# Performance work log

Hardware: AMD Instinct MI355X
Metric: run time of the kernel (lower is better)

Reference implementation:

```python
import jax, jax.numpy as jnp
import numpy as np

B, DIM, IMG, HEADS, DH = 8, 512, 32, 8, 64
INNER = HEADS * DH  # == DIM, required by final reshape(b, n, c)
N = IMG * IMG
BN_EPS = 1e-5


def setup_inputs() -> dict:
    key = jax.random.key(0)
    ks = jax.random.split(key, 11)
    s = lambda k, sh: jax.random.normal(k, sh, jnp.float32) * 0.05
    return {
        "x": jax.random.normal(ks[0], (B, N, DIM), jnp.float32),
        # stacked q/k/v params, index 0=q, 1=k, 2=v
        "dw_w": s(ks[1], (3, DIM, 1, 3, 3)),   # depthwise conv kernels (OIHW, groups=DIM)
        "dw_b": s(ks[2], (3, DIM)),
        "bn_g": jnp.ones((3, DIM), jnp.float32) + s(ks[3], (3, DIM)),
        "bn_b": s(ks[4], (3, DIM)),
        "bn_m": s(ks[5], (3, DIM)),
        "bn_v": jnp.abs(jax.random.normal(ks[6], (3, DIM), jnp.float32)) + 1.0,
        "pw_w": s(ks[7], (3, INNER, DIM)),     # pointwise 1x1 conv weights
        "pw_b": s(ks[8], (3, INNER)),
        "out_w": s(ks[9], (DIM, INNER)),       # nn.Linear weight [out, in]
        "out_b": s(ks[10], (DIM,)),
    }


def _proj(x_img, dw_w, dw_b, bn_g, bn_b, bn_m, bn_v, pw_w, pw_b):
    # depthwise 3x3 conv, stride 1, pad 1
    y = jax.lax.conv_general_dilated(
        x_img, dw_w, (1, 1), [(1, 1), (1, 1)],
        dimension_numbers=("NCHW", "OIHW", "NCHW"), feature_group_count=DIM)
    y = y + dw_b[None, :, None, None]
    # eval-mode BatchNorm2d
    scale = bn_g / jnp.sqrt(bn_v + BN_EPS)
    y = (y - bn_m[None, :, None, None]) * scale[None, :, None, None] + bn_b[None, :, None, None]
    # pointwise 1x1 conv
    y = jnp.einsum("bchw,oc->bohw", y, pw_w) + pw_b[None, :, None, None]
    return y


def reference(x, dw_w, dw_b, bn_g, bn_b, bn_m, bn_v, pw_w, pw_b, out_w, out_b):
    b = x.shape[0]
    # b (l w) c -> b c l w
    xi = x.transpose(0, 2, 1).reshape(b, DIM, IMG, IMG)
    # q, k, v: b (h d) l w -> b h (l w) d
    qkv = [
        _proj(xi, dw_w[i], dw_b[i], bn_g[i], bn_b[i], bn_m[i], bn_v[i], pw_w[i], pw_b[i])
        .reshape(b, HEADS, DH, N).transpose(0, 1, 3, 2)
        for i in range(3)
    ]
    q, k, v = qkv
    att = jax.nn.softmax(jnp.einsum("bhnd,bhmd->bhnm", q, k) * (DH ** -0.5), axis=-1)
    out = jnp.einsum("bhnm,bhmd->bhnd", att, v)  # [b,h,n,d]
    out = out.transpose(0, 2, 1, 3).reshape(b, N, INNER)
    return out @ out_w.T + out_b  # to_out Linear (dropout=0)
```

## Files before the change

### kernel.cpp

```cpp
#include <hip/hip_runtime.h>
#include <hip/hip_bf16.h>

#define BB    8
#define DIMC  512
#define IMGS  32
#define NPIX  1024
#define NHEAD 8
#define DHEAD 64

typedef __attribute__((ext_vector_type(8))) short short8;
typedef __attribute__((ext_vector_type(4))) float float4v;

__device__ __forceinline__ float b2f(unsigned short u) {
  union { unsigned int i; float f; } c;
  c.i = ((unsigned int)u) << 16;
  return c.f;
}
__device__ __forceinline__ unsigned short f2b(float f) {
  union { float f; unsigned int u; } c;
  c.f = f;
  unsigned int r = c.u + 0x7fffu + ((c.u >> 16) & 1u);
  return (unsigned short)(r >> 16);
}

__device__ __forceinline__ void storeC(float* p, float v) { *p = v; }
__device__ __forceinline__ void storeC(unsigned short* p, float v) { *p = f2b(v); }

__device__ __forceinline__ void async16(const void* g, void* l) {
  __builtin_amdgcn_global_load_lds(
      (const __attribute__((address_space(1))) void*)g,
      (__attribute__((address_space(3))) void*)l, 16, 0, 0);
}

#define WAITCNT_VM0   0x0F70
#define WAITCNT_LGKM0 0xC07F

__global__ __launch_bounds__(256) void wcvt_kernel(
    const float* __restrict__ pw_w, const float* __restrict__ out_w,
    const float* __restrict__ pw_b, const float* __restrict__ dw_w,
    const float* __restrict__ dw_b, const float* __restrict__ bn_g,
    const float* __restrict__ bn_b, const float* __restrict__ bn_m,
    const float* __restrict__ bn_v, unsigned short* __restrict__ wbf,
    float* __restrict__ bb, float* __restrict__ wT,
    float* __restrict__ shiftv) {
  const int i4 = (blockIdx.x * 256 + threadIdx.x) * 4;
  float4 v = (i4 < 3 * DIMC * DIMC)
                 ? *reinterpret_cast<const float4*>(pw_w + i4)
                 : *reinterpret_cast<const float4*>(out_w + (i4 - 3 * DIMC * DIMC));
  const float sc = (i4 < DIMC * DIMC) ? 0.125f : 1.0f;
  ushort4 o;
  o.x = f2b(v.x * sc); o.y = f2b(v.y * sc); o.z = f2b(v.z * sc); o.w = f2b(v.w * sc);
  *reinterpret_cast<ushort4*>(wbf + i4) = o;
  const int idx = blockIdx.x * 256 + threadIdx.x;
  if (idx < 6 * 256) {
    if (idx < 3 * DIMC / 2) {
      #pragma unroll
      for (int hh = 0; hh < 2; ++hh) {
        const int id2 = idx * 2 + hh;
        const int i = id2 >> 9, c = id2 & 511;
        const float scale = bn_g[id2] * rsqrtf(bn_v[id2] + 1e-5f);
        shiftv[id2] = (dw_b[id2] - bn_m[id2]) * scale + bn_b[id2];
        #pragma unroll
        for (int t = 0; t < 9; ++t)
          wT[(i * 9 + t) * DIMC + c] = dw_w[(size_t)id2 * 9 + t] * scale;
      }
    }
    #pragma unroll
    for (int k = 0; k < 1; ++k) {
      if (idx < 3 * DIMC)
        bb[idx] = pw_b[idx] * (idx < DIMC ? 0.125f : 1.0f);
    }
  }
}

__global__ __launch_bounds__(256) void dwbn_kernel(
    const float* __restrict__ x, const float* __restrict__ wT,
    const float* __restrict__ shiftv, unsigned short* __restrict__ z) {
  const int wp = blockIdx.x, lg = blockIdx.y, b = blockIdx.z;
  const int t = threadIdx.x;
  const int c = (t & 127) * 4;
  const int w = wp * 2 + (t >> 7);
  const int l0 = lg * 4;
  const float* xb = x + (size_t)b * NPIX * DIMC + c;

  const float4 zero4 = make_float4(0.f, 0.f, 0.f, 0.f);
  float4 win[6][3];
  #pragma unroll
  for (int rr = 0; rr < 6; ++rr) {
    const int l = l0 - 1 + rr;
    #pragma unroll
    for (int dw = 0; dw < 3; ++dw) {
      const int ww = w - 1 + dw;
      const bool ok = ((unsigned)l < IMGS) && ((unsigned)ww < IMGS);
      win[rr][dw] = ok ? *reinterpret_cast<const float4*>(
                             xb + (size_t)(l * IMGS + ww) * DIMC)
                       : zero4;
    }
  }

  #pragma unroll
  for (int i = 0; i < 3; ++i) {
    float4 wv[9];
    #pragma unroll
    for (int tp = 0; tp < 9; ++tp)
      wv[tp] = *reinterpret_cast<const float4*>(wT + (i * 9 + tp) * DIMC + c);
    const float4 sh = *reinterpret_cast<const float4*>(shiftv + i * DIMC + c);
    #pragma unroll
    for (int r = 0; r < 4; ++r) {
      float a0 = sh.x, a1 = sh.y, a2 = sh.z, a3 = sh.w;
      #pragma unroll
      for (int kh = 0; kh < 3; ++kh)
        #pragma unroll
        for (int kw = 0; kw < 3; ++kw) {
          const float4 wq = wv[kh * 3 + kw];
          const float4 xq = win[r + kh][kw];
          a0 = fmaf(wq.x, xq.x, a0);
          a1 = fmaf(wq.y, xq.y, a1);
          a2 = fmaf(wq.z, xq.z, a2);
          a3 = fmaf(wq.w, xq.w, a3);
        }
      ushort4 st;
      st.x = f2b(a0); st.y = f2b(a1); st.z = f2b(a2); st.w = f2b(a3);
      *reinterpret_cast<ushort4*>(
          z + (((size_t)(i * BB + b)) * NPIX + (l0 + r) * IMGS + w) * DIMC + c) = st;
    }
  }
}

template <typename CT>
__global__ __launch_bounds__(256) void gemm_mfma(
    const unsigned short* __restrict__ Abase,
    const unsigned short* __restrict__ Wbase,
    const float* __restrict__ biasBase, CT* __restrict__ Cbase) {
  __shared__ short As[8 * 64 * 8];
  __shared__ short Bs[8 * 64 * 8];
  const int bz = blockIdx.z;
  const int wi = bz >> 3;
  const short* A = (const short*)Abase + (size_t)bz * NPIX * DIMC;
  const short* W = (const short*)Wbase + (size_t)wi * DIMC * DIMC;
  const float* bias = biasBase + wi * DIMC;
  CT* C = Cbase + (size_t)bz * NPIX * DIMC;

  const int t = threadIdx.x;
  const int wv = t >> 6, lane = t & 63;
  const int lo = lane & 15, hi = lane >> 4;
  const int wm = wv >> 1, wn = wv & 1;
  const int m0 = blockIdx.y * 128, n0 = blockIdx.x * 128;

  float4v acc[4][4];
  #pragma unroll
  for (int i = 0; i < 4; ++i)
    #pragma unroll
    for (int j = 0; j < 4; ++j) acc[i][j] = {0.f, 0.f, 0.f, 0.f};

  for (int k0 = 0; k0 < DIMC; k0 += 32) {
    #pragma unroll
    for (int p = 0; p < 2; ++p) {
      const int sub = wv + p * 4;
      async16(A + (size_t)(m0 + sub * 16 + lo) * DIMC + k0 + hi * 8,
              As + (sub * 64 + lane) * 8);
      async16(W + (size_t)(n0 + sub * 16 + lo) * DIMC + k0 + hi * 8,
              Bs + (sub * 64 + lane) * 8);
    }
    __syncthreads();
    short8 af[4], bf[4];
    #pragma unroll
    for (int mt = 0; mt < 4; ++mt)
      af[mt] = *reinterpret_cast<const short8*>(As + ((wm * 4 + mt) * 64 + lane) * 8);
    #pragma unroll
    for (int nt = 0; nt < 4; ++nt)
      bf[nt] = *reinterpret_cast<const short8*>(Bs + ((wn * 4 + nt) * 64 + lane) * 8);
    #pragma unroll
    for (int mt = 0; mt < 4; ++mt)
      #pragma unroll
      for (int nt = 0; nt < 4; ++nt)
        acc[mt][nt] = __builtin_amdgcn_mfma_f32_16x16x32_bf16(af[mt], bf[nt],
                                                              acc[mt][nt], 0, 0, 0);
    __syncthreads();
  }

  float bv[4];
  #pragma unroll
  for (int nt = 0; nt < 4; ++nt) bv[nt] = bias[n0 + wn * 64 + nt * 16 + lo];
  #pragma unroll
  for (int mt = 0; mt < 4; ++mt) {
    #pragma unroll
    for (int r = 0; r < 4; ++r) {
      const int row = m0 + wm * 64 + mt * 16 + hi * 4 + r;
      CT* cp = C + (size_t)row * DIMC + n0 + wn * 64 + lo;
      #pragma unroll
      for (int nt = 0; nt < 4; ++nt) storeC(cp + nt * 16, acc[mt][nt][r] + bv[nt]);
    }
  }
}

__global__ __launch_bounds__(256) void vt_kernel(
    const unsigned short* __restrict__ v, unsigned short* __restrict__ vt) {
  __shared__ unsigned short tile[64][68];
  const int n0 = blockIdx.x * 64, h = blockIdx.y, b = blockIdx.z;
  const int t = threadIdx.x;
  const unsigned short* vb = v + (size_t)b * NPIX * DIMC + h * DHEAD;
  #pragma unroll
  for (int u = 0; u < 4; ++u) {
    const int lin = t + u * 256;
    const int row = lin >> 4, c4 = (lin & 15) * 4;
    *reinterpret_cast<ushort4*>(&tile[row][c4]) =
        *reinterpret_cast<const ushort4*>(vb + (size_t)(n0 + row) * DIMC + c4);
  }
  __syncthreads();
  unsigned short* vtb = vt + ((size_t)(b * NHEAD + h)) * DHEAD * NPIX;
  #pragma unroll
  for (int u = 0; u < 4; ++u) {
    const int lin = t + u * 256;
    const int d = lin >> 4, n4 = (lin & 15) * 4;
    ushort4 o;
    o.x = tile[n4 + 0][d];
    o.y = tile[n4 + 1][d];
    o.z = tile[n4 + 2][d];
    o.w = tile[n4 + 3][d];
    *reinterpret_cast<ushort4*>(vtb + (size_t)d * NPIX + n0 + n4) = o;
  }
}

__global__ __launch_bounds__(256, 2) void attn_mfma(
    const unsigned short* __restrict__ qkv, const unsigned short* __restrict__ vt,
    unsigned short* __restrict__ attn_o) {
  __shared__ char sm[53248];
  const int qt = blockIdx.x, h = blockIdx.y, b = blockIdx.z;
  const int t = threadIdx.x;
  const int wv = t >> 6, lane = t & 63;
  const int lo = lane & 15, hi = lane >> 4;

  char* wbase = sm + wv * 13312;
  short* Ks = (short*)(wbase);
  short* VTs = (short*)(wbase + 4096);
  short* Ps = (short*)(wbase + 8192);

  const short* qb = (const short*)qkv + ((size_t)(0 * BB + b) * NPIX) * DIMC + h * DHEAD;
  const short* kb = (const short*)qkv + ((size_t)(1 * BB + b) * NPIX) * DIMC + h * DHEAD;
  const short* vtb = (const short*)vt + ((size_t)(b * NHEAD + h)) * DHEAD * NPIX;

  short8 qf[4][2];
  #pragma unroll
  for (int mt = 0; mt < 4; ++mt)
    #pragma unroll
    for (int cc = 0; cc < 2; ++cc)
      qf[mt][cc] = *reinterpret_cast<const short8*>(
          qb + (size_t)(qt * 64 + mt * 16 + lo) * DIMC + cc * 32 + hi * 8);

  float4v oacc[4][4];
  float4v lsum[4];
  #pragma unroll
  for (int mt = 0; mt < 4; ++mt) {
    lsum[mt] = {0.f, 0.f, 0.f, 0.f};
    #pragma unroll
    for (int dt = 0; dt < 4; ++dt) oacc[mt][dt] = {0.f, 0.f, 0.f, 0.f};
  }

  const int n0 = wv * 256;
  for (int kt = 0; kt < 8; ++kt) {
    const int kbase = n0 + kt * 32;
    __builtin_amdgcn_s_waitcnt(WAITCNT_LGKM0);
    __builtin_amdgcn_sched_barrier(0);
    #pragma unroll
    for (int s = 0; s < 4; ++s) {
      const int nt = s >> 1, cc = s & 1;
      async16(kb + (size_t)(kbase + nt * 16 + lo) * DIMC + cc * 32 + hi * 8,
              Ks + (s * 64 + lane) * 8);
    }
    #pragma unroll
    for (int dt = 0; dt < 4; ++dt)
      async16(vtb + (size_t)(dt * 16 + lo) * NPIX + kbase + hi * 8,
              VTs + (dt * 64 + lane) * 8);
    __builtin_amdgcn_sched_barrier(0);
    __builtin_amdgcn_s_waitcnt(WAITCNT_VM0);
    __builtin_amdgcn_sched_barrier(0);

    short8 kf[2][2];
    #pragma unroll
    for (int nt = 0; nt < 2; ++nt)
      #pragma unroll
      for (int cc = 0; cc < 2; ++cc)
        kf[nt][cc] = *reinterpret_cast<const short8*>(Ks + ((nt * 2 + cc) * 64 + lane) * 8);
    float4v sacc[4][2];
    #pragma unroll
    for (int mt = 0; mt < 4; ++mt)
      #pragma unroll
      for (int nt = 0; nt < 2; ++nt) {
        sacc[mt][nt] = {0.f, 0.f, 0.f, 0.f};
        sacc[mt][nt] = __builtin_amdgcn_mfma_f32_16x16x32_bf16(qf[mt][0], kf[nt][0],
                                                               sacc[mt][nt], 0, 0, 0);
        sacc[mt][nt] = __builtin_amdgcn_mfma_f32_16x16x32_bf16(qf[mt][1], kf[nt][1],
                                                               sacc[mt][nt], 0, 0, 0);
      }

    #pragma unroll
    for (int mt = 0; mt < 4; ++mt)
      #pragma unroll
      for (int nt = 0; nt < 2; ++nt)
        #pragma unroll
        for (int r = 0; r < 4; ++r) {
          const float p = __expf(sacc[mt][nt][r]);
          Ps[(mt * 16 + hi * 4 + r) * 40 + nt * 16 + lo] = (short)f2b(p);
          lsum[mt][r] += p;
        }

    short8 vf[4];
    #pragma unroll
    for (int dt = 0; dt < 4; ++dt)
      vf[dt] = *reinterpret_cast<const short8*>(VTs + (dt * 64 + lane) * 8);
    #pragma unroll
    for (int mt = 0; mt < 4; ++mt) {
      const short8 pf = *reinterpret_cast<const short8*>(Ps + (mt * 16 + lo) * 40 + hi * 8);
      #pragma unroll
      for (int dt = 0; dt < 4; ++dt)
        oacc[mt][dt] = __builtin_amdgcn_mfma_f32_16x16x32_bf16(pf, vf[dt],
                                                               oacc[mt][dt], 0, 0, 0);
    }
  }

  #pragma unroll
  for (int mt = 0; mt < 4; ++mt)
    #pragma unroll
    for (int r = 0; r < 4; ++r) {
      float v = lsum[mt][r];
      v += __shfl_xor(v, 1);
      v += __shfl_xor(v, 2);
      v += __shfl_xor(v, 4);
      v += __shfl_xor(v, 8);
      lsum[mt][r] = v;
    }

  float* Obuf = (float*)sm;
  float* lbuf = (float*)(sm + 16384);
  float* linv = (float*)(sm + 17408);
  __syncthreads();
  if (lo == 0) {
    #pragma unroll
    for (int mt = 0; mt < 4; ++mt)
      #pragma unroll
      for (int r = 0; r < 4; ++r) lbuf[wv * 64 + mt * 16 + hi * 4 + r] = lsum[mt][r];
  }
  __syncthreads();
  if (t < 64) linv[t] = 1.0f / (lbuf[t] + lbuf[64 + t] + lbuf[128 + t] + lbuf[192 + t]);

  unsigned short* aob = attn_o + ((size_t)b * NPIX + qt * 64) * DIMC + h * DHEAD;
  #pragma unroll
  for (int mt = 0; mt < 4; ++mt) {
    __syncthreads();
    #pragma unroll
    for (int dt = 0; dt < 4; ++dt)
      #pragma unroll
      for (int r = 0; r < 4; ++r)
        Obuf[wv * 1024 + (dt * 4 + r) * 64 + lane] = oacc[mt][dt][r];
    __syncthreads();
    #pragma unroll
    for (int k2 = 0; k2 < 4; ++k2) {
      const int e = t + k2 * 256;
      const float sum2 = Obuf[e] + Obuf[1024 + e] + Obuf[2048 + e] + Obuf[3072 + e];
      const int dt = e >> 8, r = (e >> 6) & 3, le = e & 63;
      const int row = mt * 16 + (le >> 4) * 4 + r, d = dt * 16 + (le & 15);
      aob[(size_t)row * DIMC + d] = f2b(sum2 * linv[row]);
    }
  }
}

extern "C" void kernel_launch(void* const* d_in, const int* in_sizes, int n_in,
                              void* d_out, int out_size, void* d_ws, size_t ws_size,
                              hipStream_t stream) {
  const float* x    = (const float*)d_in[0];
  const float* dw_w = (const float*)d_in[1];
  const float* dw_b = (const float*)d_in[2];
  const float* bn_g = (const float*)d_in[3];
  const float* bn_b = (const float*)d_in[4];
  const float* bn_m = (const float*)d_in[5];
  const float* bn_v = (const float*)d_in[6];
  const float* pw_w = (const float*)d_in[7];
  const float* pw_b = (const float*)d_in[8];
  const float* out_w = (const float*)d_in[9];
  const float* out_b = (const float*)d_in[10];
  float* out = (float*)d_out;

  unsigned short* z   = (unsigned short*)d_ws;
  unsigned short* qkv = z + (size_t)3 * BB * NPIX * DIMC;
  unsigned short* wbf = qkv + (size_t)3 * BB * NPIX * DIMC;
  float* bb = (float*)(wbf + (size_t)4 * DIMC * DIMC);
  float* wT = bb + 3 * DIMC;
  float* shiftv = wT + 3 * 9 * DIMC;
  unsigned short* vtb = z;
  unsigned short* attn_o = z + (size_t)BB * NHEAD * DHEAD * NPIX;

  wcvt_kernel<<<dim3(1024), 256, 0, stream>>>(pw_w, out_w, pw_b, dw_w, dw_b,
                                              bn_g, bn_b, bn_m, bn_v, wbf, bb,
                                              wT, shiftv);
  dwbn_kernel<<<dim3(16, 8, BB), 256, 0, stream>>>(x, wT, shiftv, z);
  gemm_mfma<unsigned short><<<dim3(4, 8, 24), 256, 0, stream>>>(z, wbf, bb, qkv);
  vt_kernel<<<dim3(16, NHEAD, BB), 256, 0, stream>>>(
      qkv + (size_t)2 * BB * NPIX * DIMC, vtb);
  attn_mfma<<<dim3(16, NHEAD, BB), 256, 0, stream>>>(qkv, vtb, attn_o);
  gemm_mfma<float><<<dim3(4, 8, 8), 256, 0, stream>>>(
      attn_o, wbf + (size_t)3 * DIMC * DIMC, out_b, out);
}
```

Measured before the change: 204.2 us.

## Keep softmax probabilities in registers via transposed S and fp16 PV MFMA

```diff
diff --git a/kernel.cpp b/kernel.cpp
--- a/kernel.cpp
+++ b/kernel.cpp
@@ -10,6 +10,8 @@
 
 typedef __attribute__((ext_vector_type(8))) short short8;
 typedef __attribute__((ext_vector_type(4))) float float4v;
+typedef __attribute__((ext_vector_type(2))) _Float16 half2v;
+typedef __attribute__((ext_vector_type(4))) _Float16 half4v;
 
 __device__ __forceinline__ float b2f(unsigned short u) {
   union { unsigned int i; float f; } c;
@@ -22,6 +24,11 @@
   unsigned int r = c.u + 0x7fffu + ((c.u >> 16) & 1u);
   return (unsigned short)(r >> 16);
 }
+__device__ __forceinline__ unsigned short f2h(float f) {
+  union { _Float16 h; unsigned short u; } c;
+  c.h = (_Float16)f;
+  return c.u;
+}
 
 __device__ __forceinline__ void storeC(float* p, float v) { *p = v; }
 __device__ __forceinline__ void storeC(unsigned short* p, float v) { *p = f2b(v); }
@@ -31,9 +38,6 @@
       (const __attribute__((address_space(1))) void*)g,
       (__attribute__((address_space(3))) void*)l, 16, 0, 0);
 }
-
-#define WAITCNT_VM0   0x0F70
-#define WAITCNT_LGKM0 0xC07F
 
 __global__ __launch_bounds__(256) void wcvt_kernel(
     const float* __restrict__ pw_w, const float* __restrict__ out_w,
@@ -65,11 +69,8 @@
           wT[(i * 9 + t) * DIMC + c] = dw_w[(size_t)id2 * 9 + t] * scale;
       }
     }
-    #pragma unroll
-    for (int k = 0; k < 1; ++k) {
-      if (idx < 3 * DIMC)
-        bb[idx] = pw_b[idx] * (idx < DIMC ? 0.125f : 1.0f);
-    }
+    if (idx < 3 * DIMC)
+      bb[idx] = pw_b[idx] * (idx < DIMC ? 0.125f : 1.0f);
   }
 }
 
@@ -214,31 +215,27 @@
     const int lin = t + u * 256;
     const int d = lin >> 4, n4 = (lin & 15) * 4;
     ushort4 o;
-    o.x = tile[n4 + 0][d];
-    o.y = tile[n4 + 1][d];
-    o.z = tile[n4 + 2][d];
-    o.w = tile[n4 + 3][d];
+    o.x = f2h(b2f(tile[n4 + 0][d]));
+    o.y = f2h(b2f(tile[n4 + 1][d]));
+    o.z = f2h(b2f(tile[n4 + 2][d]));
+    o.w = f2h(b2f(tile[n4 + 3][d]));
     *reinterpret_cast<ushort4*>(vtb + (size_t)d * NPIX + n0 + n4) = o;
   }
 }
 
-__global__ __launch_bounds__(256, 2) void attn_mfma(
+__global__ __launch_bounds__(256, 3) void attn_mfma(
     const unsigned short* __restrict__ qkv, const unsigned short* __restrict__ vt,
     unsigned short* __restrict__ attn_o) {
-  __shared__ char sm[53248];
-  const int qt = blockIdx.x, h = blockIdx.y, b = blockIdx.z;
+  __shared__ char sm[17664];
+  const int b = blockIdx.x, h = blockIdx.y, qt = blockIdx.z;
   const int t = threadIdx.x;
   const int wv = t >> 6, lane = t & 63;
   const int lo = lane & 15, hi = lane >> 4;
 
-  char* wbase = sm + wv * 13312;
-  short* Ks = (short*)(wbase);
-  short* VTs = (short*)(wbase + 4096);
-  short* Ps = (short*)(wbase + 8192);
-
   const short* qb = (const short*)qkv + ((size_t)(0 * BB + b) * NPIX) * DIMC + h * DHEAD;
   const short* kb = (const short*)qkv + ((size_t)(1 * BB + b) * NPIX) * DIMC + h * DHEAD;
-  const short* vtb = (const short*)vt + ((size_t)(b * NHEAD + h)) * DHEAD * NPIX;
+  const _Float16* vth =
+      (const _Float16*)vt + ((size_t)(b * NHEAD + h)) * DHEAD * NPIX;
 
   short8 qf[4][2];
   #pragma unroll
@@ -249,97 +246,70 @@
           qb + (size_t)(qt * 64 + mt * 16 + lo) * DIMC + cc * 32 + hi * 8);
 
   float4v oacc[4][4];
-  float4v lsum[4];
+  float lsumv[4] = {0.f, 0.f, 0.f, 0.f};
+  #pragma unroll
+  for (int mt = 0; mt < 4; ++mt)
+    #pragma unroll
+    for (int dt = 0; dt < 4; ++dt) oacc[mt][dt] = {0.f, 0.f, 0.f, 0.f};
+
+  const int kw0 = wv * 256;
+  for (int it = 0; it < 16; ++it) {
+    const int k0 = kw0 + it * 16;
+    const short8 kf0 =
+        *reinterpret_cast<const short8*>(kb + (size_t)(k0 + lo) * DIMC + hi * 8);
+    const short8 kf1 =
+        *reinterpret_cast<const short8*>(kb + (size_t)(k0 + lo) * DIMC + 32 + hi * 8);
+    half4v vf[4];
+    #pragma unroll
+    for (int dt = 0; dt < 4; ++dt)
+      vf[dt] = *reinterpret_cast<const half4v*>(
+          vth + (size_t)(dt * 16 + lo) * NPIX + k0 + hi * 4);
+
+    float4v sacc[4];
+    #pragma unroll
+    for (int mt = 0; mt < 4; ++mt) {
+      sacc[mt] = {0.f, 0.f, 0.f, 0.f};
+      sacc[mt] = __builtin_amdgcn_mfma_f32_16x16x32_bf16(kf0, qf[mt][0], sacc[mt], 0, 0, 0);
+      sacc[mt] = __builtin_amdgcn_mfma_f32_16x16x32_bf16(kf1, qf[mt][1], sacc[mt], 0, 0, 0);
+    }
+
+    half4v pf[4];
+    #pragma unroll
+    for (int mt = 0; mt < 4; ++mt) {
+      const float p0 = __expf(sacc[mt][0]);
+      const float p1 = __expf(sacc[mt][1]);
+      const float p2 = __expf(sacc[mt][2]);
+      const float p3 = __expf(sacc[mt][3]);
+      lsumv[mt] += (p0 + p1) + (p2 + p3);
+      const half2v a01 =
+          __builtin_bit_cast(half2v, __builtin_amdgcn_cvt_pkrtz(p0, p1));
+      const half2v a23 =
+          __builtin_bit_cast(half2v, __builtin_amdgcn_cvt_pkrtz(p2, p3));
+      pf[mt] = half4v{a01[0], a01[1], a23[0], a23[1]};
+    }
+
+    #pragma unroll
+    for (int mt = 0; mt < 4; ++mt)
+      #pragma unroll
+      for (int dt = 0; dt < 4; ++dt)
+        oacc[mt][dt] = __builtin_amdgcn_mfma_f32_16x16x16f16(pf[mt], vf[dt],
+                                                             oacc[mt][dt], 0, 0, 0);
+  }
+
   #pragma unroll
   for (int mt = 0; mt < 4; ++mt) {
-    lsum[mt] = {0.f, 0.f, 0.f, 0.f};
-    #pragma unroll
-    for (int dt = 0; dt < 4; ++dt) oacc[mt][dt] = {0.f, 0.f, 0.f, 0.f};
-  }
-
-  const int n0 = wv * 256;
-  for (int kt = 0; kt < 8; ++kt) {
-    const int kbase = n0 + kt * 32;
-    __builtin_amdgcn_s_waitcnt(WAITCNT_LGKM0);
-    __builtin_amdgcn_sched_barrier(0);
-    #pragma unroll
-    for (int s = 0; s < 4; ++s) {
-      const int nt = s >> 1, cc = s & 1;
-      async16(kb + (size_t)(kbase + nt * 16 + lo) * DIMC + cc * 32 + hi * 8,
-              Ks + (s * 64 + lane) * 8);
-    }
-    #pragma unroll
-    for (int dt = 0; dt < 4; ++dt)
-      async16(vtb + (size_t)(dt * 16 + lo) * NPIX + kbase + hi * 8,
-              VTs + (dt * 64 + lane) * 8);
-    __builtin_amdgcn_sched_barrier(0);
-    __builtin_amdgcn_s_waitcnt(WAITCNT_VM0);
-    __builtin_amdgcn_sched_barrier(0);
-
-    short8 kf[2][2];
-    #pragma unroll
-    for (int nt = 0; nt < 2; ++nt)
-      #pragma unroll
-      for (int cc = 0; cc < 2; ++cc)
-        kf[nt][cc] = *reinterpret_cast<const short8*>(Ks + ((nt * 2 + cc) * 64 + lane) * 8);
-    float4v sacc[4][2];
-    #pragma unroll
-    for (int mt = 0; mt < 4; ++mt)
-      #pragma unroll
-      for (int nt = 0; nt < 2; ++nt) {
-        sacc[mt][nt] = {0.f, 0.f, 0.f, 0.f};
-        sacc[mt][nt] = __builtin_amdgcn_mfma_f32_16x16x32_bf16(qf[mt][0], kf[nt][0],
-                                                               sacc[mt][nt], 0, 0, 0);
-        sacc[mt][nt] = __builtin_amdgcn_mfma_f32_16x16x32_bf16(qf[mt][1], kf[nt][1],
-                                                               sacc[mt][nt], 0, 0, 0);
-      }
-
-    #pragma unroll
-    for (int mt = 0; mt < 4; ++mt)
-      #pragma unroll
-      for (int nt = 0; nt < 2; ++nt)
-        #pragma unroll
-        for (int r = 0; r < 4; ++r) {
-          const float p = __expf(sacc[mt][nt][r]);
-          Ps[(mt * 16 + hi * 4 + r) * 40 + nt * 16 + lo] = (short)f2b(p);
-          lsum[mt][r] += p;
-        }
-
-    short8 vf[4];
-    #pragma unroll
-    for (int dt = 0; dt < 4; ++dt)
-      vf[dt] = *reinterpret_cast<const short8*>(VTs + (dt * 64 + lane) * 8);
-    #pragma unroll
-    for (int mt = 0; mt < 4; ++mt) {
-      const short8 pf = *reinterpret_cast<const short8*>(Ps + (mt * 16 + lo) * 40 + hi * 8);
-      #pragma unroll
-      for (int dt = 0; dt < 4; ++dt)
-        oacc[mt][dt] = __builtin_amdgcn_mfma_f32_16x16x32_bf16(pf, vf[dt],
-                                                               oacc[mt][dt], 0, 0, 0);
-    }
-  }
-
-  #pragma unroll
-  for (int mt = 0; mt < 4; ++mt)
-    #pragma unroll
-    for (int r = 0; r < 4; ++r) {
-      float v = lsum[mt][r];
-      v += __shfl_xor(v, 1);
-      v += __shfl_xor(v, 2);
-      v += __shfl_xor(v, 4);
-      v += __shfl_xor(v, 8);
-      lsum[mt][r] = v;
-    }
+    float v = lsumv[mt];
+    v += __shfl_xor(v, 16);
+    v += __shfl_xor(v, 32);
+    lsumv[mt] = v;
+  }
 
   float* Obuf = (float*)sm;
   float* lbuf = (float*)(sm + 16384);
   float* linv = (float*)(sm + 17408);
-  __syncthreads();
-  if (lo == 0) {
-    #pragma unroll
-    for (int mt = 0; mt < 4; ++mt)
-      #pragma unroll
-      for (int r = 0; r < 4; ++r) lbuf[wv * 64 + mt * 16 + hi * 4 + r] = lsum[mt][r];
+  if (hi == 0) {
+    #pragma unroll
+    for (int mt = 0; mt < 4; ++mt) lbuf[wv * 64 + mt * 16 + lo] = lsumv[mt];
   }
   __syncthreads();
   if (t < 64) linv[t] = 1.0f / (lbuf[t] + lbuf[64 + t] + lbuf[128 + t] + lbuf[192 + t]);
@@ -397,7 +367,7 @@
   gemm_mfma<unsigned short><<<dim3(4, 8, 24), 256, 0, stream>>>(z, wbf, bb, qkv);
   vt_kernel<<<dim3(16, NHEAD, BB), 256, 0, stream>>>(
       qkv + (size_t)2 * BB * NPIX * DIMC, vtb);
-  attn_mfma<<<dim3(16, NHEAD, BB), 256, 0, stream>>>(qkv, vtb, attn_o);
+  attn_mfma<<<dim3(BB, NHEAD, 16), 256, 0, stream>>>(qkv, vtb, attn_o);
   gemm_mfma<float><<<dim3(4, 8, 8), 256, 0, stream>>>(
       attn_o, wbf + (size_t)3 * DIMC * DIMC, out_b, out);
 }
```

Measured after the change: 215.5 us. 5.6% more time.
